# Kernel optimization log

Hardware: AMD Instinct MI355X
Metric: run time of the kernel (lower is better)

The kernel has to match this reference:

```python
import jax, jax.numpy as jnp
import numpy as np

D_MODEL = 2048
NUM_HEADS = 32
HEAD_DIM = D_MODEL // NUM_HEADS  # 64
ROPE_BASE = 10000.0


def _rope_cos_sin(seq_len, head_dim, dtype):
    inv_freq = 1.0 / (ROPE_BASE ** (jnp.arange(0, head_dim, 2, dtype=jnp.float32) / head_dim))
    freqs = jnp.arange(seq_len, dtype=jnp.float32)[:, None] * inv_freq[None, :]  # (S, Dh/2)
    emb = jnp.concatenate([freqs, freqs], axis=-1)  # (S, Dh)
    return emb.astype(dtype), jnp.cos(emb).astype(dtype), jnp.sin(emb).astype(dtype)


def _rotate_half(x):
    x1, x2 = jnp.split(x, 2, axis=-1)
    return jnp.concatenate([-x2, x1], axis=-1)


def setup_inputs() -> dict:
    key = jax.random.key(0)
    k1, k2, k3, k4 = jax.random.split(key, 4)
    B, S, D = 1, 2048, D_MODEL
    x = jax.random.normal(k1, (B, S, D), dtype=jnp.float32)
    Wqkv = jax.random.normal(k2, (3 * D, D), dtype=jnp.float32) * 0.02
    Wo = jax.random.normal(k3, (D, D), dtype=jnp.float32) * 0.02
    gate = jax.random.normal(k4, (D,), dtype=jnp.float32) * 0.1
    return {"x": x, "Wqkv": Wqkv, "Wo": Wo, "gate": gate}


def reference(x, Wqkv, Wo, gate):
    B, S, D = x.shape
    H, Dh = NUM_HEADS, HEAD_DIM
    residual = x

    # fused QKV projection (torch Linear: y = x @ W.T)
    qkv = jnp.einsum('bsd,ed->bse', x, Wqkv).reshape(B, S, 3, H, Dh)
    q, k, v = qkv[:, :, 0], qkv[:, :, 1], qkv[:, :, 2]  # each (B, S, H, Dh)

    # RoPE
    _, cos, sin = _rope_cos_sin(S, Dh, x.dtype)
    cos = cos[None, :, None, :]  # (1, S, 1, Dh)
    sin = sin[None, :, None, :]
    q = q * cos + _rotate_half(q) * sin
    k = k * cos + _rotate_half(k) * sin

    # causal SDPA
    scale = 1.0 / np.sqrt(Dh)
    scores = jnp.einsum('bqhd,bkhd->bhqk', q, k) * scale  # (B, H, S, S)
    causal = jnp.tril(jnp.ones((S, S), dtype=bool))
    scores = jnp.where(causal[None, None], scores, jnp.finfo(scores.dtype).min)
    probs = jax.nn.softmax(scores, axis=-1)
    attn = jnp.einsum('bhqk,bkhd->bqhd', probs, v).reshape(B, S, D)

    out = jnp.einsum('bsd,ed->bse', attn, Wo)
    # HeoGate: learned per-channel gated residual (assumption; see notes)
    return residual + gate * out
```

## Files before the change

### kernel.cpp

```cpp
#include <hip/hip_runtime.h>
#include <hip/hip_bf16.h>
#include <cstdint>
#include <cstddef>

typedef __hip_bfloat16 bf16;
typedef short short8 __attribute__((ext_vector_type(8)));
typedef float f32x4 __attribute__((ext_vector_type(4)));

#define S_LEN 2048
#define DMODEL 2048
#define NQKV 6144
#define NHEADS 32
#define HDIM 64
#define ROPE_L2 0.4152410118609203f

__device__ __forceinline__ void async_copy16(const bf16* g, bf16* l) {
  __builtin_amdgcn_global_load_lds(
      (const __attribute__((address_space(1))) void*)g,
      (__attribute__((address_space(3))) void*)l, 16, 0, 0);
}

__device__ __forceinline__ f32x4 mfma_bf16(short8 a, short8 b, f32x4 c) {
  return __builtin_amdgcn_mfma_f32_16x16x32_bf16(a, b, c, 0, 0, 0);
}

__global__ __launch_bounds__(256) void cvt3_kernel(const float* __restrict__ sx,
                                                   bf16* __restrict__ dx,
                                                   const float* __restrict__ sw,
                                                   bf16* __restrict__ dw,
                                                   const float* __restrict__ so,
                                                   bf16* __restrict__ dov) {
  int i = blockIdx.x * 256 + threadIdx.x;
  const float* s;
  bf16* d;
  if (i < 1048576) {
    s = sx; d = dx;
  } else if (i < 4194304) {
    s = sw; d = dw; i -= 1048576;
  } else {
    s = so; d = dov; i -= 4194304;
  }
  const float4 v = ((const float4*)s)[i];
  union { bf16 h[4]; ushort4 u; } tmp;
  tmp.h[0] = __float2bfloat16(v.x);
  tmp.h[1] = __float2bfloat16(v.y);
  tmp.h[2] = __float2bfloat16(v.z);
  tmp.h[3] = __float2bfloat16(v.w);
  ((ushort4*)d)[i] = tmp.u;
}

__global__ __launch_bounds__(256) void gemm_qkv(const bf16* __restrict__ A,
                                                const bf16* __restrict__ W,
                                                bf16* __restrict__ q_ws,
                                                bf16* __restrict__ k_ws,
                                                bf16* __restrict__ v_ws) {
  constexpr int K = DMODEL;
  __shared__ bf16 smem[8192];
  const int tid = threadIdx.x;
  const int wave = tid >> 6, lane = tid & 63;
  const int wm = wave >> 1, wn = wave & 1;
  const int m0 = blockIdx.y * 128, n0 = blockIdx.x * 128;
  const int sr = wave * 16 + (lane >> 2);
  const int swc = (((lane & 3) ^ ((lane >> 3) & 3)) * 8);
  const int fr = lane & 15, fq = lane >> 4;
  const int rdc = ((fq ^ ((fr >> 1) & 3)) * 8);

  const f32x4 zero = {0.f, 0.f, 0.f, 0.f};
  f32x4 acc[4][4];
  for (int i = 0; i < 4; ++i)
    for (int j = 0; j < 4; ++j) acc[i][j] = zero;

  for (int kt = 0; kt < K; kt += 32) {
    __syncthreads();
    for (int i2 = 0; i2 < 2; ++i2) {
      async_copy16(A + (size_t)(m0 + i2 * 64 + sr) * K + kt + swc,
                   &smem[(i2 * 64 + wave * 16) * 32]);
      async_copy16(W + (size_t)(n0 + i2 * 64 + sr) * K + kt + swc,
                   &smem[4096 + (i2 * 64 + wave * 16) * 32]);
    }
    __syncthreads();
    short8 a[4], b[4];
    for (int i = 0; i < 4; ++i)
      a[i] = *(const short8*)&smem[(wm * 64 + i * 16 + fr) * 32 + rdc];
    for (int j = 0; j < 4; ++j)
      b[j] = *(const short8*)&smem[4096 + (wn * 64 + j * 16 + fr) * 32 + rdc];
    for (int i = 0; i < 4; ++i)
      for (int j = 0; j < 4; ++j)
        acc[i][j] = mfma_bf16(a[i], b[j], acc[i][j]);
  }

  const int colb = n0 + wn * 64;
  const int sect = colb >> 11;
  const int h = (colb & 2047) >> 6;
  const int col = fr, rq = fq * 4;

  if (sect < 2) {
    bf16* dst = ((sect == 0) ? q_ws : k_ws) + (size_t)h * S_LEN * HDIM;
    bf16* rep = smem + wave * 1152;
    const float f0 = exp2f(-(float)col * ROPE_L2);
    const float f1 = exp2f(-(float)(16 + col) * ROPE_L2);
    __syncthreads();
    for (int i = 0; i < 4; ++i) {
      const int base_s = m0 + wm * 64 + i * 16;
#pragma unroll
      for (int jl = 0; jl < 2; ++jl) {
        const int dh = jl * 16 + col;
        const float fr_ = (jl == 0) ? f0 : f1;
#pragma unroll
        for (int r = 0; r < 4; ++r) {
          const int srow = base_s + rq + r;
          float sn, cs;
          __sincosf((float)srow * fr_, &sn, &cs);
          const float xl = acc[i][jl][r], xh = acc[i][jl + 2][r];
          rep[(rq + r) * 72 + dh]      = __float2bfloat16(xl * cs - xh * sn);
          rep[(rq + r) * 72 + dh + 32] = __float2bfloat16(xh * cs + xl * sn);
        }
      }
#pragma unroll
      for (int p = 0; p < 2; ++p) {
        const int rr = p * 8 + (lane >> 3), ch = lane & 7;
        const uint4 vv = *(const uint4*)&rep[rr * 72 + ch * 8];
        *(uint4*)&dst[(size_t)(base_s + rr) * HDIM + ch * 8] = vv;
      }
    }
  } else {
    bf16* dst = v_ws + (size_t)h * HDIM * S_LEN;
    for (int j = 0; j < 4; ++j) {
      const int dh = j * 16 + col;
      for (int i = 0; i < 4; ++i) {
        const int s0 = m0 + wm * 64 + i * 16 + rq;
        union { bf16 hx[4]; uint2 u; } vk;
#pragma unroll
        for (int r = 0; r < 4; ++r) vk.hx[r] = __float2bfloat16(acc[i][j][r]);
        *(uint2*)&dst[(size_t)dh * S_LEN + s0] = vk.u;
      }
    }
  }
}

__global__ __launch_bounds__(256) void attn_kernel(const bf16* __restrict__ q_ws,
                                                   const bf16* __restrict__ k_ws,
                                                   const bf16* __restrict__ vt_ws,
                                                   bf16* __restrict__ attn_out) {
  const int bid = blockIdx.x;
  const int qt = 31 - (bid >> 5);
  const int h = bid & 31;

  const int tid = threadIdx.x, wave = tid >> 6, lane = tid & 63;
  const int col = lane & 15, fq = lane >> 4;
  const int q_glob = qt * 64 + wave * 16 + col;

  __shared__ bf16 Ks[2][64 * 64];
  __shared__ bf16 Vs[2][64 * 64];
  __shared__ bf16 Pl[4][16 * 72];
  bf16* pl = Pl[wave];

  const bf16* qh = q_ws + (size_t)h * S_LEN * HDIM;
  const bf16* kh = k_ws + (size_t)h * S_LEN * HDIM;
  const bf16* vh = vt_ws + (size_t)h * HDIM * S_LEN;

  const int srow = lane >> 3;
  const int slot = lane & 7;
  const int schunk = slot ^ srow;

  auto stage = [&](int kt, int buf) {
    const int k0 = kt * 64;
#pragma unroll
    for (int j = 0; j < 2; ++j) {
      const int r8 = (wave * 2 + j) * 8;
      async_copy16(kh + (size_t)(k0 + r8 + srow) * HDIM + schunk * 8,
                   &Ks[buf][r8 * 64]);
      async_copy16(vh + (size_t)(r8 + srow) * S_LEN + k0 + schunk * 8,
                   &Vs[buf][r8 * 64]);
    }
  };

  short8 qf[2];
#pragma unroll
  for (int ks = 0; ks < 2; ++ks)
    qf[ks] = *(const short8*)&qh[(size_t)q_glob * HDIM + ks * 32 + fq * 8];

  const f32x4 zero = {0.f, 0.f, 0.f, 0.f};
  f32x4 o_acc[4] = {zero, zero, zero, zero};
  float m_i = -1e30f, l_i = 0.f;

  stage(0, 0);

  for (int kt = 0; kt <= qt; ++kt) {
    const int buf = kt & 1;
    const int k0 = kt * 64;
    __syncthreads();
    if (kt < qt) stage(kt + 1, buf ^ 1);

    short8 kf[8];
#pragma unroll
    for (int n = 0; n < 4; ++n) {
      const int row = n * 16 + col;
#pragma unroll
      for (int ks = 0; ks < 2; ++ks)
        kf[n * 2 + ks] =
            *(const short8*)&Ks[buf][row * 64 + (((ks * 4 + fq) ^ (row & 7)) * 8)];
    }
    f32x4 s_acc[4] = {zero, zero, zero, zero};
#pragma unroll
    for (int n = 0; n < 4; ++n)
#pragma unroll
      for (int ks = 0; ks < 2; ++ks)
        s_acc[n] = mfma_bf16(kf[n * 2 + ks], qf[ks], s_acc[n]);

    short8 vf[8];
#pragma unroll
    for (int n = 0; n < 4; ++n) {
      const int row = n * 16 + col;
#pragma unroll
      for (int ks = 0; ks < 2; ++ks)
        vf[n * 2 + ks] =
            *(const short8*)&Vs[buf][row * 64 + (((ks * 4 + fq) ^ (row & 7)) * 8)];
    }

    if (kt == qt) {
#pragma unroll
      for (int n = 0; n < 4; ++n)
#pragma unroll
        for (int r = 0; r < 4; ++r)
          if (k0 + n * 16 + fq * 4 + r > q_glob) s_acc[n][r] = -1e30f;
    }

    float vmax = -1e30f;
#pragma unroll
    for (int n = 0; n < 4; ++n)
#pragma unroll
      for (int r = 0; r < 4; ++r) vmax = fmaxf(vmax, s_acc[n][r]);
    vmax = fmaxf(vmax, __shfl_xor(vmax, 16, 64));
    vmax = fmaxf(vmax, __shfl_xor(vmax, 32, 64));
    const float mnew = fmaxf(m_i, vmax);
    const float alpha = __expf((m_i - mnew) * 0.125f);
    m_i = mnew;

    float rs = 0.f;
#pragma unroll
    for (int n = 0; n < 4; ++n)
#pragma unroll
      for (int r = 0; r < 4; ++r) {
        const float p = __expf((s_acc[n][r] - mnew) * 0.125f);
        s_acc[n][r] = p;
        rs += p;
      }
    rs += __shfl_xor(rs, 16, 64);
    rs += __shfl_xor(rs, 32, 64);
    l_i = l_i * alpha + rs;

#pragma unroll
    for (int n = 0; n < 4; ++n)
#pragma unroll
      for (int r = 0; r < 4; ++r) o_acc[n][r] *= alpha;

#pragma unroll
    for (int n = 0; n < 4; ++n) {
      union { bf16 hx[4]; uint2 u; } pk;
#pragma unroll
      for (int r = 0; r < 4; ++r) pk.hx[r] = __float2bfloat16(s_acc[n][r]);
      *(uint2*)&pl[col * 72 + n * 16 + fq * 4] = pk.u;
    }
    short8 pa[2];
#pragma unroll
    for (int ks = 0; ks < 2; ++ks)
      pa[ks] = *(const short8*)&pl[col * 72 + ks * 32 + fq * 8];

#pragma unroll
    for (int n = 0; n < 4; ++n)
#pragma unroll
      for (int ks = 0; ks < 2; ++ks)
        o_acc[n] = mfma_bf16(vf[n * 2 + ks], pa[ks], o_acc[n]);
  }

  const float inv = 1.0f / l_i;
#pragma unroll
  for (int n = 0; n < 4; ++n) {
#pragma unroll
    for (int r = 0; r < 4; ++r) o_acc[n][r] *= inv;
    union { bf16 hx[4]; uint2 u; } ok;
#pragma unroll
    for (int r = 0; r < 4; ++r) ok.hx[r] = __float2bfloat16(o_acc[n][r]);
    *(uint2*)&attn_out[(size_t)q_glob * DMODEL + h * HDIM + n * 16 + fq * 4] = ok.u;
  }
}

__global__ __launch_bounds__(256) void gemm_out(const bf16* __restrict__ A,
                                                const bf16* __restrict__ W,
                                                const float* __restrict__ xres,
                                                const float* __restrict__ gate,
                                                float* __restrict__ out) {
  constexpr int K = DMODEL;
  __shared__ bf16 As[64 * 32];
  __shared__ bf16 Bs[128 * 32];
  const int tid = threadIdx.x;
  const int wave = tid >> 6, lane = tid & 63;
  const int m0 = blockIdx.y * 64, n0 = blockIdx.x * 128;
  const int sr = lane >> 2;
  const int swc = (((lane & 3) ^ ((lane >> 3) & 3)) * 8);
  const int fr = lane & 15, fq = lane >> 4;
  const int rdc = ((fq ^ ((fr >> 1) & 3)) * 8);

  const f32x4 zero = {0.f, 0.f, 0.f, 0.f};
  f32x4 acc[4][2];
  for (int i = 0; i < 4; ++i)
    for (int j = 0; j < 2; ++j) acc[i][j] = zero;

  for (int kt = 0; kt < K; kt += 32) {
    __syncthreads();
    async_copy16(A + (size_t)(m0 + wave * 16 + sr) * K + kt + swc,
                 &As[(wave * 16) * 32]);
#pragma unroll
    for (int j = 0; j < 2; ++j)
      async_copy16(W + (size_t)(n0 + wave * 32 + j * 16 + sr) * K + kt + swc,
                   &Bs[(wave * 32 + j * 16) * 32]);
    __syncthreads();
    short8 a[4], b[2];
    for (int i = 0; i < 4; ++i)
      a[i] = *(const short8*)&As[(i * 16 + fr) * 32 + rdc];
    for (int j = 0; j < 2; ++j)
      b[j] = *(const short8*)&Bs[(wave * 32 + j * 16 + fr) * 32 + rdc];
    for (int i = 0; i < 4; ++i)
      for (int j = 0; j < 2; ++j)
        acc[i][j] = mfma_bf16(a[i], b[j], acc[i][j]);
  }

  const int col = fr, rq = fq * 4;
  for (int j = 0; j < 2; ++j) {
    const int cc = n0 + wave * 32 + j * 16 + col;
    const float g = gate[cc];
    for (int i = 0; i < 4; ++i) {
      const int base_row = m0 + i * 16 + rq;
      for (int r = 0; r < 4; ++r) {
        const size_t idx = (size_t)(base_row + r) * DMODEL + cc;
        out[idx] = xres[idx] + g * acc[i][j][r];
      }
    }
  }
}

extern "C" void kernel_launch(void* const* d_in, const int* in_sizes, int n_in,
                              void* d_out, int out_size, void* d_ws, size_t ws_size,
                              hipStream_t stream) {
  const float* x    = (const float*)d_in[0];
  const float* Wqkv = (const float*)d_in[1];
  const float* Wo   = (const float*)d_in[2];
  const float* gate = (const float*)d_in[3];
  float* out = (float*)d_out;

  char* ws = (char*)d_ws;
  const size_t MB = 1024 * 1024;
  bf16* xb      = (bf16*)(ws);
  bf16* wqkvb   = (bf16*)(ws + 8 * MB);
  bf16* wob     = (bf16*)(ws + 32 * MB);
  bf16* q_ws    = (bf16*)(ws + 40 * MB);
  bf16* k_ws    = (bf16*)(ws + 48 * MB);
  bf16* v_ws    = (bf16*)(ws + 56 * MB);
  bf16* attn_ws = (bf16*)(ws);

  cvt3_kernel<<<dim3(20480), 256, 0, stream>>>(x, xb, Wqkv, wqkvb, Wo, wob);

  gemm_qkv<<<dim3(NQKV / 128, DMODEL / 128), 256, 0, stream>>>(xb, wqkvb, q_ws, k_ws, v_ws);
  attn_kernel<<<dim3(1024), 256, 0, stream>>>(q_ws, k_ws, v_ws, attn_ws);
  gemm_out<<<dim3(DMODEL / 128, DMODEL / 64), 256, 0, stream>>>(attn_ws, wob, x, gate, out);
}
```

Baseline: 253.1 us.

## Double attention query tile per block and deepen GEMM K-step to 64

The attention kernel now gives each block 128 queries (two 16-row query groups per wave) instead of 64. Each staged K/V tile is reused across twice as many queries, and the grid is halved to 512 blocks. Both GEMMs load a 64-wide K slab per iteration into larger shared buffers, halving the number of barrier pairs. The costs are more registers and LDS per block, fewer attention blocks for load balancing, and some masked wasted work on the diagonal tiles.

After: 283.5 us. +12.0%, slower.

```diff
diff --git a/kernel.cpp b/kernel.cpp
--- a/kernel.cpp
+++ b/kernel.cpp
@@ -55,7 +55,7 @@
                                                 bf16* __restrict__ k_ws,
                                                 bf16* __restrict__ v_ws) {
   constexpr int K = DMODEL;
-  __shared__ bf16 smem[8192];
+  __shared__ bf16 smem[16384];
   const int tid = threadIdx.x;
   const int wave = tid >> 6, lane = tid & 63;
   const int wm = wave >> 1, wn = wave & 1;
@@ -70,23 +70,34 @@
   for (int i = 0; i < 4; ++i)
     for (int j = 0; j < 4; ++j) acc[i][j] = zero;
 
-  for (int kt = 0; kt < K; kt += 32) {
+  for (int kt = 0; kt < K; kt += 64) {
     __syncthreads();
     for (int i2 = 0; i2 < 2; ++i2) {
-      async_copy16(A + (size_t)(m0 + i2 * 64 + sr) * K + kt + swc,
-                   &smem[(i2 * 64 + wave * 16) * 32]);
-      async_copy16(W + (size_t)(n0 + i2 * 64 + sr) * K + kt + swc,
-                   &smem[4096 + (i2 * 64 + wave * 16) * 32]);
-    }
-    __syncthreads();
-    short8 a[4], b[4];
-    for (int i = 0; i < 4; ++i)
-      a[i] = *(const short8*)&smem[(wm * 64 + i * 16 + fr) * 32 + rdc];
-    for (int j = 0; j < 4; ++j)
-      b[j] = *(const short8*)&smem[4096 + (wn * 64 + j * 16 + fr) * 32 + rdc];
-    for (int i = 0; i < 4; ++i)
+      const size_t ra = (size_t)(m0 + i2 * 64 + sr) * K + kt;
+      const size_t rw = (size_t)(n0 + i2 * 64 + sr) * K + kt;
+      const int db = (i2 * 64 + wave * 16) * 32;
+      async_copy16(A + ra + swc,        &smem[db]);
+      async_copy16(A + ra + 32 + swc,   &smem[4096 + db]);
+      async_copy16(W + rw + swc,        &smem[8192 + db]);
+      async_copy16(W + rw + 32 + swc,   &smem[12288 + db]);
+    }
+    __syncthreads();
+#pragma unroll
+    for (int kk = 0; kk < 2; ++kk) {
+      const int ab = kk * 4096, wb = 8192 + kk * 4096;
+      short8 a[4], b[4];
+#pragma unroll
+      for (int i = 0; i < 4; ++i)
+        a[i] = *(const short8*)&smem[ab + (wm * 64 + i * 16 + fr) * 32 + rdc];
+#pragma unroll
       for (int j = 0; j < 4; ++j)
-        acc[i][j] = mfma_bf16(a[i], b[j], acc[i][j]);
+        b[j] = *(const short8*)&smem[wb + (wn * 64 + j * 16 + fr) * 32 + rdc];
+#pragma unroll
+      for (int i = 0; i < 4; ++i)
+#pragma unroll
+        for (int j = 0; j < 4; ++j)
+          acc[i][j] = mfma_bf16(a[i], b[j], acc[i][j]);
+    }
   }
 
   const int colb = n0 + wn * 64;
@@ -143,16 +154,19 @@
                                                    const bf16* __restrict__ vt_ws,
                                                    bf16* __restrict__ attn_out) {
   const int bid = blockIdx.x;
-  const int qt = 31 - (bid >> 5);
+  const int t = 15 - (bid >> 5);
   const int h = bid & 31;
+  const int qb = t * 128;
+  const int nkt = 2 * t + 2;
 
   const int tid = threadIdx.x, wave = tid >> 6, lane = tid & 63;
   const int col = lane & 15, fq = lane >> 4;
-  const int q_glob = qt * 64 + wave * 16 + col;
+  const int q0g = qb + wave * 32 + col;
+  const int q1g = q0g + 16;
 
   __shared__ bf16 Ks[2][64 * 64];
   __shared__ bf16 Vs[2][64 * 64];
-  __shared__ bf16 Pl[4][16 * 72];
+  __shared__ bf16 Pl[4][32 * 72];
   bf16* pl = Pl[wave];
 
   const bf16* qh = q_ws + (size_t)h * S_LEN * HDIM;
@@ -175,22 +189,26 @@
     }
   };
 
-  short8 qf[2];
-#pragma unroll
-  for (int ks = 0; ks < 2; ++ks)
-    qf[ks] = *(const short8*)&qh[(size_t)q_glob * HDIM + ks * 32 + fq * 8];
+  short8 qf[2][2];
+#pragma unroll
+  for (int g = 0; g < 2; ++g)
+#pragma unroll
+    for (int ks = 0; ks < 2; ++ks)
+      qf[g][ks] =
+          *(const short8*)&qh[(size_t)(q0g + g * 16) * HDIM + ks * 32 + fq * 8];
 
   const f32x4 zero = {0.f, 0.f, 0.f, 0.f};
-  f32x4 o_acc[4] = {zero, zero, zero, zero};
-  float m_i = -1e30f, l_i = 0.f;
+  f32x4 o0[4] = {zero, zero, zero, zero};
+  f32x4 o1[4] = {zero, zero, zero, zero};
+  float m0v = -1e30f, l0v = 0.f, m1v = -1e30f, l1v = 0.f;
 
   stage(0, 0);
 
-  for (int kt = 0; kt <= qt; ++kt) {
+  for (int kt = 0; kt < nkt; ++kt) {
     const int buf = kt & 1;
     const int k0 = kt * 64;
     __syncthreads();
-    if (kt < qt) stage(kt + 1, buf ^ 1);
+    if (kt + 1 < nkt) stage(kt + 1, buf ^ 1);
 
     short8 kf[8];
 #pragma unroll
@@ -201,12 +219,15 @@
         kf[n * 2 + ks] =
             *(const short8*)&Ks[buf][row * 64 + (((ks * 4 + fq) ^ (row & 7)) * 8)];
     }
-    f32x4 s_acc[4] = {zero, zero, zero, zero};
+    f32x4 s0[4] = {zero, zero, zero, zero};
+    f32x4 s1[4] = {zero, zero, zero, zero};
 #pragma unroll
     for (int n = 0; n < 4; ++n)
 #pragma unroll
-      for (int ks = 0; ks < 2; ++ks)
-        s_acc[n] = mfma_bf16(kf[n * 2 + ks], qf[ks], s_acc[n]);
+      for (int ks = 0; ks < 2; ++ks) {
+        s0[n] = mfma_bf16(kf[n * 2 + ks], qf[0][ks], s0[n]);
+        s1[n] = mfma_bf16(kf[n * 2 + ks], qf[1][ks], s1[n]);
+      }
 
     short8 vf[8];
 #pragma unroll
@@ -218,71 +239,113 @@
             *(const short8*)&Vs[buf][row * 64 + (((ks * 4 + fq) ^ (row & 7)) * 8)];
     }
 
-    if (kt == qt) {
+    if (k0 + 63 > qb + wave * 32) {
 #pragma unroll
       for (int n = 0; n < 4; ++n)
 #pragma unroll
         for (int r = 0; r < 4; ++r)
-          if (k0 + n * 16 + fq * 4 + r > q_glob) s_acc[n][r] = -1e30f;
-    }
-
-    float vmax = -1e30f;
+          if (k0 + n * 16 + fq * 4 + r > q0g) s0[n][r] = -1e30f;
+    }
+    if (k0 + 63 > qb + wave * 32 + 16) {
+#pragma unroll
+      for (int n = 0; n < 4; ++n)
+#pragma unroll
+        for (int r = 0; r < 4; ++r)
+          if (k0 + n * 16 + fq * 4 + r > q1g) s1[n][r] = -1e30f;
+    }
+
+    {
+      float vmax = -1e30f;
+#pragma unroll
+      for (int n = 0; n < 4; ++n)
+#pragma unroll
+        for (int r = 0; r < 4; ++r) vmax = fmaxf(vmax, s0[n][r]);
+      vmax = fmaxf(vmax, __shfl_xor(vmax, 16, 64));
+      vmax = fmaxf(vmax, __shfl_xor(vmax, 32, 64));
+      const float mnew = fmaxf(m0v, vmax);
+      const float alpha = __expf((m0v - mnew) * 0.125f);
+      m0v = mnew;
+      float rs = 0.f;
+#pragma unroll
+      for (int n = 0; n < 4; ++n)
+#pragma unroll
+        for (int r = 0; r < 4; ++r) {
+          const float p = __expf((s0[n][r] - mnew) * 0.125f);
+          s0[n][r] = p;
+          rs += p;
+        }
+      rs += __shfl_xor(rs, 16, 64);
+      rs += __shfl_xor(rs, 32, 64);
+      l0v = l0v * alpha + rs;
+#pragma unroll
+      for (int n = 0; n < 4; ++n) {
+#pragma unroll
+        for (int r = 0; r < 4; ++r) o0[n][r] *= alpha;
+        union { bf16 hx[4]; uint2 u; } pk;
+#pragma unroll
+        for (int r = 0; r < 4; ++r) pk.hx[r] = __float2bfloat16(s0[n][r]);
+        *(uint2*)&pl[col * 72 + n * 16 + fq * 4] = pk.u;
+      }
+    }
+    {
+      float vmax = -1e30f;
+#pragma unroll
+      for (int n = 0; n < 4; ++n)
+#pragma unroll
+        for (int r = 0; r < 4; ++r) vmax = fmaxf(vmax, s1[n][r]);
+      vmax = fmaxf(vmax, __shfl_xor(vmax, 16, 64));
+      vmax = fmaxf(vmax, __shfl_xor(vmax, 32, 64));
+      const float mnew = fmaxf(m1v, vmax);
+      const float alpha = __expf((m1v - mnew) * 0.125f);
+      m1v = mnew;
+      float rs = 0.f;
+#pragma unroll
+      for (int n = 0; n < 4; ++n)
+#pragma unroll
+        for (int r = 0; r < 4; ++r) {
+          const float p = __expf((s1[n][r] - mnew) * 0.125f);
+          s1[n][r] = p;
+          rs += p;
+        }
+      rs += __shfl_xor(rs, 16, 64);
+      rs += __shfl_xor(rs, 32, 64);
+      l1v = l1v * alpha + rs;
+#pragma unroll
+      for (int n = 0; n < 4; ++n) {
+#pragma unroll
+        for (int r = 0; r < 4; ++r) o1[n][r] *= alpha;
+        union { bf16 hx[4]; uint2 u; } pk;
+#pragma unroll
+        for (int r = 0; r < 4; ++r) pk.hx[r] = __float2bfloat16(s1[n][r]);
+        *(uint2*)&pl[(16 + col) * 72 + n * 16 + fq * 4] = pk.u;
+      }
+    }
+
+    short8 pa0[2], pa1[2];
+#pragma unroll
+    for (int ks = 0; ks < 2; ++ks) {
+      pa0[ks] = *(const short8*)&pl[col * 72 + ks * 32 + fq * 8];
+      pa1[ks] = *(const short8*)&pl[(16 + col) * 72 + ks * 32 + fq * 8];
+    }
 #pragma unroll
     for (int n = 0; n < 4; ++n)
 #pragma unroll
-      for (int r = 0; r < 4; ++r) vmax = fmaxf(vmax, s_acc[n][r]);
-    vmax = fmaxf(vmax, __shfl_xor(vmax, 16, 64));
-    vmax = fmaxf(vmax, __shfl_xor(vmax, 32, 64));
-    const float mnew = fmaxf(m_i, vmax);
-    const float alpha = __expf((m_i - mnew) * 0.125f);
-    m_i = mnew;
-
-    float rs = 0.f;
-#pragma unroll
-    for (int n = 0; n < 4; ++n)
-#pragma unroll
-      for (int r = 0; r < 4; ++r) {
-        const float p = __expf((s_acc[n][r] - mnew) * 0.125f);
-        s_acc[n][r] = p;
-        rs += p;
-      }
-    rs += __shfl_xor(rs, 16, 64);
-    rs += __shfl_xor(rs, 32, 64);
-    l_i = l_i * alpha + rs;
-
-#pragma unroll
-    for (int n = 0; n < 4; ++n)
-#pragma unroll
-      for (int r = 0; r < 4; ++r) o_acc[n][r] *= alpha;
-
-#pragma unroll
-    for (int n = 0; n < 4; ++n) {
-      union { bf16 hx[4]; uint2 u; } pk;
-#pragma unroll
-      for (int r = 0; r < 4; ++r) pk.hx[r] = __float2bfloat16(s_acc[n][r]);
-      *(uint2*)&pl[col * 72 + n * 16 + fq * 4] = pk.u;
-    }
-    short8 pa[2];
-#pragma unroll
-    for (int ks = 0; ks < 2; ++ks)
-      pa[ks] = *(const short8*)&pl[col * 72 + ks * 32 + fq * 8];
-
-#pragma unroll
-    for (int n = 0; n < 4; ++n)
-#pragma unroll
-      for (int ks = 0; ks < 2; ++ks)
-        o_acc[n] = mfma_bf16(vf[n * 2 + ks], pa[ks], o_acc[n]);
-  }
-
-  const float inv = 1.0f / l_i;
+      for (int ks = 0; ks < 2; ++ks) {
+        o0[n] = mfma_bf16(vf[n * 2 + ks], pa0[ks], o0[n]);
+        o1[n] = mfma_bf16(vf[n * 2 + ks], pa1[ks], o1[n]);
+      }
+  }
+
+  const float inv0 = 1.0f / l0v, inv1 = 1.0f / l1v;
 #pragma unroll
   for (int n = 0; n < 4; ++n) {
-#pragma unroll
-    for (int r = 0; r < 4; ++r) o_acc[n][r] *= inv;
     union { bf16 hx[4]; uint2 u; } ok;
 #pragma unroll
-    for (int r = 0; r < 4; ++r) ok.hx[r] = __float2bfloat16(o_acc[n][r]);
-    *(uint2*)&attn_out[(size_t)q_glob * DMODEL + h * HDIM + n * 16 + fq * 4] = ok.u;
+    for (int r = 0; r < 4; ++r) ok.hx[r] = __float2bfloat16(o0[n][r] * inv0);
+    *(uint2*)&attn_out[(size_t)q0g * DMODEL + h * HDIM + n * 16 + fq * 4] = ok.u;
+#pragma unroll
+    for (int r = 0; r < 4; ++r) ok.hx[r] = __float2bfloat16(o1[n][r] * inv1);
+    *(uint2*)&attn_out[(size_t)q1g * DMODEL + h * HDIM + n * 16 + fq * 4] = ok.u;
   }
 }
 
@@ -292,8 +355,7 @@
                                                 const float* __restrict__ gate,
                                                 float* __restrict__ out) {
   constexpr int K = DMODEL;
-  __shared__ bf16 As[64 * 32];
-  __shared__ bf16 Bs[128 * 32];
+  __shared__ bf16 smem[12288];
   const int tid = threadIdx.x;
   const int wave = tid >> 6, lane = tid & 63;
   const int m0 = blockIdx.y * 64, n0 = blockIdx.x * 128;
@@ -307,23 +369,37 @@
   for (int i = 0; i < 4; ++i)
     for (int j = 0; j < 2; ++j) acc[i][j] = zero;
 
-  for (int kt = 0; kt < K; kt += 32) {
-    __syncthreads();
-    async_copy16(A + (size_t)(m0 + wave * 16 + sr) * K + kt + swc,
-                 &As[(wave * 16) * 32]);
-#pragma unroll
-    for (int j = 0; j < 2; ++j)
-      async_copy16(W + (size_t)(n0 + wave * 32 + j * 16 + sr) * K + kt + swc,
-                   &Bs[(wave * 32 + j * 16) * 32]);
-    __syncthreads();
-    short8 a[4], b[2];
-    for (int i = 0; i < 4; ++i)
-      a[i] = *(const short8*)&As[(i * 16 + fr) * 32 + rdc];
-    for (int j = 0; j < 2; ++j)
-      b[j] = *(const short8*)&Bs[(wave * 32 + j * 16 + fr) * 32 + rdc];
-    for (int i = 0; i < 4; ++i)
+  for (int kt = 0; kt < K; kt += 64) {
+    __syncthreads();
+    {
+      const size_t ra = (size_t)(m0 + wave * 16 + sr) * K + kt;
+      async_copy16(A + ra + swc,      &smem[(wave * 16) * 32]);
+      async_copy16(A + ra + 32 + swc, &smem[2048 + (wave * 16) * 32]);
+#pragma unroll
+      for (int j = 0; j < 2; ++j) {
+        const size_t rw = (size_t)(n0 + wave * 32 + j * 16 + sr) * K + kt;
+        const int db = (wave * 32 + j * 16) * 32;
+        async_copy16(W + rw + swc,      &smem[4096 + db]);
+        async_copy16(W + rw + 32 + swc, &smem[8192 + db]);
+      }
+    }
+    __syncthreads();
+#pragma unroll
+    for (int kk = 0; kk < 2; ++kk) {
+      const int ab = kk * 2048, wb = 4096 + kk * 4096;
+      short8 a[4], b[2];
+#pragma unroll
+      for (int i = 0; i < 4; ++i)
+        a[i] = *(const short8*)&smem[ab + (i * 16 + fr) * 32 + rdc];
+#pragma unroll
       for (int j = 0; j < 2; ++j)
-        acc[i][j] = mfma_bf16(a[i], b[j], acc[i][j]);
+        b[j] = *(const short8*)&smem[wb + (wave * 32 + j * 16 + fr) * 32 + rdc];
+#pragma unroll
+      for (int i = 0; i < 4; ++i)
+#pragma unroll
+        for (int j = 0; j < 2; ++j)
+          acc[i][j] = mfma_bf16(a[i], b[j], acc[i][j]);
+    }
   }
 
   const int col = fr, rq = fq * 4;
@@ -362,6 +438,6 @@
   cvt3_kernel<<<dim3(20480), 256, 0, stream>>>(x, xb, Wqkv, wqkvb, Wo, wob);
 
   gemm_qkv<<<dim3(NQKV / 128, DMODEL / 128), 256, 0, stream>>>(xb, wqkvb, q_ws, k_ws, v_ws);
-  attn_kernel<<<dim3(1024), 256, 0, stream>>>(q_ws, k_ws, v_ws, attn_ws);
+  attn_kernel<<<dim3(512), 256, 0, stream>>>(q_ws, k_ws, v_ws, attn_ws);
   gemm_out<<<dim3(DMODEL / 128, DMODEL / 64), 256, 0, stream>>>(attn_ws, wob, x, gate, out);
 }
```
